# Performance work log

Hardware: AMD Instinct MI355X
Metric: run time of the kernel (lower is better)

The kernel has to match this reference:

```python
import jax, jax.numpy as jnp
import numpy as np

# Model dims (see init_kwargs)
B, S, H = 1, 1024, 2048
NH, NKV, HD = 16, 4, 128       # query heads, kv heads (GQA), head dim
RD = 64                        # partial rotary dim
E, TOPK, I = 8, 2, 1024        # experts, top-k, expert intermediate
EPS = 1e-6
THETA = 1000000.0


def setup_inputs() -> dict:
    key = jax.random.key(0)
    ks = jax.random.split(key, 12)
    s = 0.02  # init scale
    return {
        "hidden_states": jax.random.normal(ks[0], (B, S, H), jnp.float32),
        "position_ids": jnp.tile(jnp.arange(S, dtype=jnp.int32), (B, 1)),
        "ln1_w": jnp.ones((H,), jnp.float32),
        "q_norm_w": jnp.ones((NH * HD,), jnp.float32),
        "k_norm_w": jnp.ones((NKV * HD,), jnp.float32),
        "wq": jax.random.normal(ks[1], (H, NH * HD), jnp.float32) * s,
        "wk": jax.random.normal(ks[2], (H, NKV * HD), jnp.float32) * s,
        "wv": jax.random.normal(ks[3], (H, NKV * HD), jnp.float32) * s,
        "wo": jax.random.normal(ks[4], (NH * HD, H), jnp.float32) * s,
        "ln2_w": jnp.ones((H,), jnp.float32),
        "router_w": jax.random.normal(ks[5], (H, E), jnp.float32) * s,
        "router_bias": jax.random.normal(ks[6], (E,), jnp.float32) * 0.1,
        "w_gate": jax.random.normal(ks[7], (E, H, I), jnp.float32) * s,
        "w_up": jax.random.normal(ks[8], (E, H, I), jnp.float32) * s,
        "w_down": jax.random.normal(ks[9], (E, I, H), jnp.float32) * s,
    }


def rmsnorm(x, w):
    # fp32 RMSNorm over full last dim (matches DistributedRMSNorm with tp=1)
    xf = x.astype(jnp.float32)
    r = jax.lax.rsqrt(jnp.mean(xf * xf, axis=-1, keepdims=True) + EPS)
    return (xf * r * w).astype(x.dtype)


def _rope(x, cos, sin):
    # partial rotary: only first RD dims of each head are rotated
    xr, xp = x[..., :RD], x[..., RD:]
    half = RD // 2
    rot = jnp.concatenate([-xr[..., half:], xr[..., :half]], axis=-1)
    return jnp.concatenate([xr * cos + rot * sin, xp], axis=-1)


def reference(hidden_states, position_ids, ln1_w, q_norm_w, k_norm_w,
              wq, wk, wv, wo, ln2_w, router_w, router_bias,
              w_gate, w_up, w_down):
    x = hidden_states
    # --- attention block ---
    h = rmsnorm(x, ln1_w)
    Q = h @ wq  # [B,S,NH*HD]
    K = h @ wk  # [B,S,NKV*HD]
    V = h @ wv
    # MiniMax M2 qk_norm: RMSNorm over FULL projection output BEFORE head reshape
    Q = rmsnorm(Q, q_norm_w)
    K = rmsnorm(K, k_norm_w)
    q = Q.reshape(B, S, NH, HD).transpose(0, 2, 1, 3)   # [B,NH,S,HD]
    k = K.reshape(B, S, NKV, HD).transpose(0, 2, 1, 3)  # [B,NKV,S,HD]
    v = V.reshape(B, S, NKV, HD).transpose(0, 2, 1, 3)
    # partial RoPE
    inv = 1.0 / (THETA ** (jnp.arange(0, RD, 2, dtype=jnp.float32) / RD))
    ang = position_ids.astype(jnp.float32)[:, :, None] * inv  # [B,S,RD/2]
    cos = jnp.concatenate([jnp.cos(ang)] * 2, axis=-1)[:, None]  # [B,1,S,RD]
    sin = jnp.concatenate([jnp.sin(ang)] * 2, axis=-1)[:, None]
    q = _rope(q, cos, sin)
    k = _rope(k, cos, sin)
    # GQA expand
    rep = NH // NKV
    k = jnp.repeat(k, rep, axis=1)
    v = jnp.repeat(v, rep, axis=1)
    scores = jnp.einsum('bhqd,bhkd->bhqk', q, k).astype(jnp.float32) / np.sqrt(HD).astype(np.float32)
    causal = jnp.tril(jnp.ones((S, S), bool))
    scores = jnp.where(causal, scores, jnp.float32(-1e30))
    attn = jax.nn.softmax(scores, axis=-1).astype(v.dtype)
    ctx = jnp.einsum('bhqk,bhkd->bhqd', attn, v)
    attn_out = ctx.transpose(0, 2, 1, 3).reshape(B, S, NH * HD) @ wo
    res = x + attn_out
    # --- MoE block ---
    h2 = rmsnorm(res, ln2_w)
    t = h2.reshape(B * S, H)
    logits = t.astype(jnp.float32) @ router_w        # [T,E]
    sc = jax.nn.sigmoid(logits)
    # top-k chosen on bias-corrected scores; weights from uncorrected scores
    _, ti = jax.lax.top_k(sc + router_bias, TOPK)    # [T,TOPK]
    aff = jnp.take_along_axis(sc, ti, axis=-1)
    aff = aff / jnp.sum(aff, axis=-1, keepdims=True)  # normalize_top_k_affinities
    T = B * S
    combine = jnp.zeros((T, E), jnp.float32).at[jnp.arange(T)[:, None], ti].add(aff)
    # SwiGLU experts (dense-compute, sparse-combine reference for blockwise grouped GEMM)
    g = jnp.einsum('th,ehi->tei', t, w_gate)
    u = jnp.einsum('th,ehi->tei', t, w_up)
    act = jax.nn.silu(g) * u
    eo = jnp.einsum('tei,eih->teh', act, w_down)
    moe = jnp.einsum('te,teh->th', combine.astype(eo.dtype), eo)
    return res + moe.reshape(B, S, H)
```

## Files before the change

kernel.cpp:

```cpp
#include <hip/hip_runtime.h>
#include <hip/hip_bf16.h>
#include <cstdint>

static constexpr int S   = 1024;
static constexpr int H   = 2048;
static constexpr int NH  = 16;
static constexpr int NKV = 4;
static constexpr int HD  = 128;
static constexpr int EXPN = 8;
static constexpr int FFI = 1024;

typedef __bf16 bf16x8 __attribute__((ext_vector_type(8)));
typedef float  f32x4  __attribute__((ext_vector_type(4)));
typedef unsigned short ushortx8 __attribute__((ext_vector_type(8)));

#define DEVI __device__ __forceinline__

DEVI unsigned short f2bf(float f) {
    union { float f; uint32_t u; } v; v.f = f;
    uint32_t r = (v.u + 0x7FFFu + ((v.u >> 16) & 1u)) >> 16;
    return (unsigned short)r;
}
DEVI float bf2f(unsigned short s) {
    union { uint32_t u; float f; } v; v.u = ((uint32_t)s) << 16; return v.f;
}

DEVI void atomAdd(float* p, float v) { unsafeAtomicAdd(p, v); }

DEVI void gll16(const unsigned short* g, unsigned short* l) {
    __builtin_amdgcn_global_load_lds(
        (const __attribute__((address_space(1))) unsigned int*)(g),
        (__attribute__((address_space(3))) unsigned int*)(l),
        16, 0, 0);
}

__global__ __launch_bounds__(256) void transT(const float* __restrict__ in,
                                              unsigned short* __restrict__ outp,
                                              int R, int C)
{
    __shared__ unsigned short tl[64][72];
    int zb = blockIdx.z;
    in   += (size_t)zb * R * C;
    outp += (size_t)zb * R * C;
    int c0 = blockIdx.x * 64, r0 = blockIdx.y * 64;
    int t = threadIdx.x;
    int cq = (t & 15) * 4;
    int rr = t >> 4;
    #pragma unroll
    for (int p = 0; p < 4; ++p) {
        int row = rr + p * 16;
        float4 v = *(const float4*)&in[(size_t)(r0 + row) * C + c0 + cq];
        tl[cq + 0][row] = f2bf(v.x);
        tl[cq + 1][row] = f2bf(v.y);
        tl[cq + 2][row] = f2bf(v.z);
        tl[cq + 3][row] = f2bf(v.w);
    }
    __syncthreads();
    int r8 = (t & 7) * 8;
    int cc = t >> 3;
    #pragma unroll
    for (int p = 0; p < 2; ++p) {
        int col = cc + p * 32;
        ushortx8 v = *(const ushortx8*)&tl[col][r8];
        *(ushortx8*)&outp[(size_t)(c0 + col) * R + r0 + r8] = v;
    }
}

enum { CFG_PROJ3 = 0, CFG_WO = 1, CFG_SCORES = 2, CFG_PV = 3, CFG_GATEUP = 4, CFG_DOWN = 5 };

template<int CFG, int WM, int NI>
__global__ __launch_bounds__(256, 2) void gemm_k(
    const unsigned short* __restrict__ A,
    const unsigned short* __restrict__ B0,
    const unsigned short* __restrict__ B1,
    const unsigned short* __restrict__ B2,
    float* __restrict__ C0,
    float* __restrict__ C1,
    float* __restrict__ C2,
    unsigned short* __restrict__ Cb,
    const float* __restrict__ X,
    const int* __restrict__ cnt,
    const int* __restrict__ tokList,
    int arg0)
{
    constexpr bool DUAL = (CFG == CFG_GATEUP);
    constexpr int BM = WM * 32;
    constexpr int BN = NI * 32;
    constexpr int ASZ = BM * 64;
    constexpr int BSZ = BN * 64;

    const int tid = threadIdx.x;
    const int m0 = blockIdx.y * BM;
    int n0 = blockIdx.x * BN;

    int M = S;
    int kbeg = 0, kend = 0, LDA = 0, LDBK = 0, LDC = 0;
    const unsigned short* Ap = A;
    const unsigned short* Bb = B0;
    const unsigned short* Bb2 = B1;
    const int* tlist = nullptr;
    float* Cout = C0;
    int head = 0, e = 0, hl = 0;

    if constexpr (CFG == CFG_PROJ3) {
        int xt = blockIdx.x;
        if (xt < 16)      { Bb = B0; Cout = C0; LDC = 2048; n0 = xt * 128; }
        else if (xt < 20) { Bb = B1; Cout = C1; LDC = 512;  n0 = (xt - 16) * 128; }
        else              { Bb = B2; Cout = C2; LDC = 512;  n0 = (xt - 20) * 128; }
        LDA = H; LDBK = H; kend = H;
    } else if constexpr (CFG == CFG_WO) {
        LDA = H; LDBK = H; LDC = H; kend = H;
    } else if constexpr (CFG == CFG_SCORES) {
        hl = blockIdx.z; head = arg0 + hl;
        if (n0 >= m0 + BM) return;
        Ap = A + (size_t)head * S * HD;
        Bb = B0 + (size_t)(head >> 2) * S * HD;
        kend = HD; LDA = HD; LDBK = HD;
    } else if constexpr (CFG == CFG_PV) {
        int z = blockIdx.z; hl = z >> 2; int ks = z & 3;
        head = arg0 + hl;
        int kcap = m0 + BM;
        kbeg = ks * 256;
        if (kbeg >= kcap) return;
        kend = (kbeg + 256 < kcap) ? kbeg + 256 : kcap;
        Ap = A + (size_t)hl * S * S;
        Bb = B0 + (size_t)(head >> 2) * HD * S;
        LDA = S; LDBK = S;
    } else if constexpr (CFG == CFG_GATEUP) {
        e = blockIdx.z;
        M = cnt[e]; if (m0 >= M) return;
        tlist = tokList + e * S;
        Bb  = B0 + (size_t)e * FFI * H;
        Bb2 = B1 + (size_t)e * FFI * H;
        kend = H; LDA = H; LDBK = H;
    } else {
        e = blockIdx.z;
        M = cnt[e]; if (m0 >= M) return;
        Ap = A + (size_t)e * S * FFI;
        Bb = B0 + (size_t)e * H * FFI;
        kend = FFI; LDA = FFI; LDBK = FFI;
    }

    __shared__ unsigned short As[2 * ASZ];
    __shared__ unsigned short Bs[2 * BSZ];
    __shared__ unsigned short Bs2[DUAL ? 2 * BSZ : 8];

    const int lane = tid & 63, grp = lane >> 4, r16 = lane & 15;
    const int wid = tid >> 6, wr = wid >> 1, wc = wid & 1;
    const int wbase8 = (tid & 0xFFC0) * 8;

    size_t aoff[WM];
    #pragma unroll
    for (int c = 0; c < WM; ++c) {
        int chunk = c * 256 + tid;
        int row = chunk >> 3;
        int kcs = (chunk & 7) * 8;
        int grow = m0 + row;
        if constexpr (CFG == CFG_GATEUP) { int r2 = grow < M ? grow : M - 1; grow = tlist[r2]; }
        else if constexpr (CFG == CFG_DOWN) { grow = grow < M ? grow : M - 1; }
        aoff[c] = (size_t)grow * LDA + (kcs ^ ((row & 7) << 3));
    }
    size_t boff[NI];
    #pragma unroll
    for (int c = 0; c < NI; ++c) {
        int chunk = c * 256 + tid;
        int row = chunk >> 3;
        int kcs = (chunk & 7) * 8;
        boff[c] = (size_t)(n0 + row) * LDBK + (kcs ^ ((row & 7) << 3));
    }

    auto STAGE = [&](int buf, int k0) {
        #pragma unroll
        for (int c = 0; c < WM; ++c)
            gll16(Ap + aoff[c] + k0, &As[buf * ASZ + c * 2048 + wbase8]);
        #pragma unroll
        for (int c = 0; c < NI; ++c)
            gll16(Bb + boff[c] + k0, &Bs[buf * BSZ + c * 2048 + wbase8]);
        if constexpr (DUAL) {
            #pragma unroll
            for (int c = 0; c < NI; ++c)
                gll16(Bb2 + boff[c] + k0, &Bs2[buf * BSZ + c * 2048 + wbase8]);
        }
    };

    f32x4 acc[WM][NI] = {};
    f32x4 acc2[DUAL ? WM : 1][DUAL ? NI : 1] = {};

    int cur = 0;
    STAGE(0, kbeg);
    __syncthreads();

    for (int k0 = kbeg; k0 < kend; k0 += 64) {
        if (k0 + 64 < kend) STAGE(cur ^ 1, k0 + 64);
        #pragma unroll
        for (int kk = 0; kk < 64; kk += 32) {
            bf16x8 af[WM], bfr[NI], bfr2[DUAL ? NI : 1];
            #pragma unroll
            for (int mi = 0; mi < WM; ++mi) {
                int r = wr * (WM * 16) + mi * 16 + r16;
                int idx = cur * ASZ + r * 64 + ((kk + grp * 8) ^ ((r & 7) << 3));
                af[mi] = __builtin_bit_cast(bf16x8, *(const ushortx8*)&As[idx]);
            }
            #pragma unroll
            for (int ni = 0; ni < NI; ++ni) {
                int r = wc * (NI * 16) + ni * 16 + r16;
                int idx = cur * BSZ + r * 64 + ((kk + grp * 8) ^ ((r & 7) << 3));
                bfr[ni] = __builtin_bit_cast(bf16x8, *(const ushortx8*)&Bs[idx]);
                if constexpr (DUAL)
                    bfr2[ni] = __builtin_bit_cast(bf16x8, *(const ushortx8*)&Bs2[idx]);
            }
            #pragma unroll
            for (int mi = 0; mi < WM; ++mi)
                #pragma unroll
                for (int ni = 0; ni < NI; ++ni) {
                    acc[mi][ni] = __builtin_amdgcn_mfma_f32_16x16x32_bf16(af[mi], bfr[ni], acc[mi][ni], 0, 0, 0);
                    if constexpr (DUAL)
                        acc2[mi][ni] = __builtin_amdgcn_mfma_f32_16x16x32_bf16(af[mi], bfr2[ni], acc2[mi][ni], 0, 0, 0);
                }
        }
        __syncthreads();
        cur ^= 1;
    }

    #pragma unroll
    for (int mi = 0; mi < WM; ++mi) {
        #pragma unroll
        for (int ni = 0; ni < NI; ++ni) {
            f32x4 v = acc[mi][ni];
            int col = n0 + wc * (NI * 16) + ni * 16 + r16;
            #pragma unroll
            for (int j = 0; j < 4; ++j) {
                int row = m0 + wr * (WM * 16) + mi * 16 + grp * 4 + j;
                float val = v[j];
                if constexpr (CFG == CFG_PROJ3) {
                    Cout[(size_t)row * LDC + col] = val;
                } else if constexpr (CFG == CFG_WO) {
                    C0[(size_t)row * H + col] = val + X[(size_t)row * H + col];
                } else if constexpr (CFG == CFG_SCORES) {
                    float sv = val * 0.08838834764831845f;
                    if (col > row) sv = -1e30f;
                    C0[((size_t)hl * S + row) * S + col] = sv;
                } else if constexpr (CFG == CFG_PV) {
                    atomAdd(&C0[(size_t)row * 2048 + head * HD + col], val);
                } else if constexpr (CFG == CFG_GATEUP) {
                    if (row < M) {
                        float g = val, u = acc2[mi][ni][j];
                        float a = g / (1.f + expf(-g)) * u;
                        Cb[((size_t)e * S + row) * FFI + col] = f2bf(a);
                    }
                } else {
                    if (row < M) {
                        Cb[((size_t)e * S + row) * H + col] = f2bf(val);
                    }
                }
            }
        }
    }
}

__global__ __launch_bounds__(256) void rms_h(const float* __restrict__ x,
                                             const float* __restrict__ w,
                                             unsigned short* __restrict__ out)
{
    int row = blockIdx.x, tid = threadIdx.x;
    const float* xr = x + (size_t)row * H;
    float4 a = *(const float4*)&xr[tid * 8];
    float4 b = *(const float4*)&xr[tid * 8 + 4];
    float vals[8] = { a.x, a.y, a.z, a.w, b.x, b.y, b.z, b.w };
    float ss = 0;
    #pragma unroll
    for (int j = 0; j < 8; ++j) ss += vals[j] * vals[j];
    __shared__ float red[4];
    #pragma unroll
    for (int o = 32; o; o >>= 1) ss += __shfl_down(ss, o);
    if ((tid & 63) == 0) red[tid >> 6] = ss;
    __syncthreads();
    float tot = red[0] + red[1] + red[2] + red[3];
    float r = rsqrtf(tot * (1.f / H) + 1e-6f);
    ushortx8 ov;
    #pragma unroll
    for (int j = 0; j < 8; ++j) ov[j] = f2bf(vals[j] * r * w[tid * 8 + j]);
    *(ushortx8*)&out[(size_t)row * H + tid * 8] = ov;
}

__global__ __launch_bounds__(256) void qnorm_rope(const float* __restrict__ qbuf,
                                                  const float* __restrict__ qw,
                                                  const int* __restrict__ pos,
                                                  unsigned short* __restrict__ qatt)
{
    int tok = blockIdx.x, tid = threadIdx.x;
    __shared__ float sh[2048];
    __shared__ float red[4];
    const float* xr = qbuf + (size_t)tok * 2048;
    float4 a = *(const float4*)&xr[tid * 8];
    float4 b = *(const float4*)&xr[tid * 8 + 4];
    *(float4*)&sh[tid * 8] = a;
    *(float4*)&sh[tid * 8 + 4] = b;
    float ss = a.x*a.x + a.y*a.y + a.z*a.z + a.w*a.w + b.x*b.x + b.y*b.y + b.z*b.z + b.w*b.w;
    #pragma unroll
    for (int o = 32; o; o >>= 1) ss += __shfl_down(ss, o);
    if ((tid & 63) == 0) red[tid >> 6] = ss;
    __syncthreads();
    float tot = red[0] + red[1] + red[2] + red[3];
    float r = rsqrtf(tot * (1.f / 2048.f) + 1e-6f);
    float p = (float)pos[tok];
    #pragma unroll
    for (int j = 0; j < 8; ++j) {
        int idx = tid * 8 + j;
        int d = idx & 127, hh = idx >> 7;
        float v = sh[idx] * r * qw[idx];
        float o;
        if (d < 64) {
            int jj = d & 31;
            float ang = p * expf((float)jj * -0.43173470268f);
            float c = cosf(ang), sn = sinf(ang);
            if (d < 32) { float v2 = sh[idx + 32] * r * qw[idx + 32]; o = v * c - v2 * sn; }
            else        { float v2 = sh[idx - 32] * r * qw[idx - 32]; o = v * c + v2 * sn; }
        } else o = v;
        qatt[((size_t)hh * S + tok) * HD + d] = f2bf(o);
    }
}

__global__ __launch_bounds__(256) void knorm_rope(const float* __restrict__ kbuf,
                                                  const float* __restrict__ kw,
                                                  const int* __restrict__ pos,
                                                  unsigned short* __restrict__ katt)
{
    int tok = blockIdx.x, tid = threadIdx.x;
    __shared__ float sh[512];
    __shared__ float red[4];
    const float* xr = kbuf + (size_t)tok * 512;
    float2 a = *(const float2*)&xr[tid * 2];
    sh[tid * 2] = a.x; sh[tid * 2 + 1] = a.y;
    float ss = a.x * a.x + a.y * a.y;
    #pragma unroll
    for (int o = 32; o; o >>= 1) ss += __shfl_down(ss, o);
    if ((tid & 63) == 0) red[tid >> 6] = ss;
    __syncthreads();
    float tot = red[0] + red[1] + red[2] + red[3];
    float r = rsqrtf(tot * (1.f / 512.f) + 1e-6f);
    float p = (float)pos[tok];
    #pragma unroll
    for (int j = 0; j < 2; ++j) {
        int idx = tid * 2 + j;
        int d = idx & 127, hh = idx >> 7;
        float v = sh[idx] * r * kw[idx];
        float o;
        if (d < 64) {
            int jj = d & 31;
            float ang = p * expf((float)jj * -0.43173470268f);
            float c = cosf(ang), sn = sinf(ang);
            if (d < 32) { float v2 = sh[idx + 32] * r * kw[idx + 32]; o = v * c - v2 * sn; }
            else        { float v2 = sh[idx - 32] * r * kw[idx - 32]; o = v * c + v2 * sn; }
        } else o = v;
        katt[((size_t)hh * S + tok) * HD + d] = f2bf(o);
    }
}

__global__ __launch_bounds__(256) void softmax_k(const float* __restrict__ scores,
                                                 unsigned short* __restrict__ pb)
{
    int bid = blockIdx.x;
    int hl = bid >> 10, q = bid & 1023;
    const float* srow = scores + ((size_t)hl * S + q) * S;
    unsigned short* prow = pb + ((size_t)hl * S + q) * S;
    int L = q + 1, tid = threadIdx.x;
    __shared__ float red[4];
    float v[4]; float mx = -3.4e38f;
    #pragma unroll
    for (int i = 0; i < 4; ++i) {
        int j = tid + i * 256;
        if (j < L) { v[i] = srow[j]; mx = fmaxf(mx, v[i]); } else v[i] = 0.f;
    }
    float m = mx;
    #pragma unroll
    for (int o = 32; o; o >>= 1) m = fmaxf(m, __shfl_down(m, o));
    if ((tid & 63) == 0) red[tid >> 6] = m;
    __syncthreads();
    float M_ = fmaxf(fmaxf(red[0], red[1]), fmaxf(red[2], red[3]));
    __syncthreads();
    float e[4]; float sum = 0;
    #pragma unroll
    for (int i = 0; i < 4; ++i) {
        int j = tid + i * 256;
        if (j < L) { e[i] = expf(v[i] - M_); sum += e[i]; } else e[i] = 0.f;
    }
    #pragma unroll
    for (int o = 32; o; o >>= 1) sum += __shfl_down(sum, o);
    if ((tid & 63) == 0) red[tid >> 6] = sum;
    __syncthreads();
    float inv = 1.f / (red[0] + red[1] + red[2] + red[3]);
    #pragma unroll
    for (int i = 0; i < 4; ++i) {
        int j = tid + i * 256;
        prow[j] = f2bf(e[i] * inv);
    }
}

__global__ void zero_cnt(int* cnt) { if (threadIdx.x < EXPN) cnt[threadIdx.x] = 0; }

__global__ void zerok(float4* __restrict__ p, int n4)
{
    int i = blockIdx.x * 256 + threadIdx.x;
    if (i < n4) p[i] = float4{0.f, 0.f, 0.f, 0.f};
}

__global__ void cvt_k(const float* __restrict__ src, unsigned short* __restrict__ dst)
{
    int i = blockIdx.x * 256 + threadIdx.x;
    float4 a = *(const float4*)&src[i * 8];
    float4 b = *(const float4*)&src[i * 8 + 4];
    float v[8] = { a.x, a.y, a.z, a.w, b.x, b.y, b.z, b.w };
    ushortx8 o;
    #pragma unroll
    for (int j = 0; j < 8; ++j) o[j] = f2bf(v[j]);
    *(ushortx8*)&dst[i * 8] = o;
}

__global__ __launch_bounds__(256) void router_k(const float* __restrict__ res,
                                                const float* __restrict__ ln2w,
                                                const float* __restrict__ rw,
                                                const float* __restrict__ rbias,
                                                int* __restrict__ cnt,
                                                int* __restrict__ tokList,
                                                int* __restrict__ slot,
                                                float* __restrict__ slotw)
{
    int tok = blockIdx.x, tid = threadIdx.x;
    const float* xr = res + (size_t)tok * H;
    float4 a = *(const float4*)&xr[tid * 8];
    float4 b = *(const float4*)&xr[tid * 8 + 4];
    float vals[8] = { a.x, a.y, a.z, a.w, b.x, b.y, b.z, b.w };
    float ss = 0;
    #pragma unroll
    for (int j = 0; j < 8; ++j) ss += vals[j] * vals[j];
    __shared__ float red[4];
    float t_ = ss;
    #pragma unroll
    for (int o = 32; o; o >>= 1) t_ += __shfl_down(t_, o);
    if ((tid & 63) == 0) red[tid >> 6] = t_;
    __syncthreads();
    float tot = red[0] + red[1] + red[2] + red[3];
    float r = rsqrtf(tot * (1.f / H) + 1e-6f);

    float acc[EXPN] = {};
    #pragma unroll
    for (int j = 0; j < 8; ++j) {
        float tv = vals[j] * r * ln2w[tid * 8 + j];
        const float* rp = rw + (size_t)(tid * 8 + j) * EXPN;
        #pragma unroll
        for (int e = 0; e < EXPN; ++e) acc[e] += tv * rp[e];
    }
    __shared__ float r8[4][EXPN];
    #pragma unroll
    for (int e = 0; e < EXPN; ++e) {
        float s_ = acc[e];
        #pragma unroll
        for (int o = 32; o; o >>= 1) s_ += __shfl_down(s_, o);
        acc[e] = s_;
    }
    if ((tid & 63) == 0)
        for (int e = 0; e < EXPN; ++e) r8[tid >> 6][e] = acc[e];
    __syncthreads();
    if (tid == 0) {
        float sg[EXPN];
        for (int e = 0; e < EXPN; ++e) {
            float lg = r8[0][e] + r8[1][e] + r8[2][e] + r8[3][e];
            sg[e] = 1.f / (1.f + expf(-lg));
        }
        int i0 = 0; float b0 = -1e30f;
        for (int e = 0; e < EXPN; ++e) {
            float s_ = sg[e] + rbias[e];
            if (s_ > b0) { b0 = s_; i0 = e; }
        }
        int i1 = -1; float b1 = -1e30f;
        for (int e = 0; e < EXPN; ++e) {
            if (e == i0) continue;
            float s_ = sg[e] + rbias[e];
            if (s_ > b1) { b1 = s_; i1 = e; }
        }
        float a0 = sg[i0], a1 = sg[i1], inv = 1.f / (a0 + a1);
        int p0 = atomicAdd(&cnt[i0], 1);
        tokList[i0 * S + p0] = tok;
        int p1 = atomicAdd(&cnt[i1], 1);
        tokList[i1 * S + p1] = tok;
        slot[tok * 2]     = i0 * S + p0;  slotw[tok * 2]     = a0 * inv;
        slot[tok * 2 + 1] = i1 * S + p1;  slotw[tok * 2 + 1] = a1 * inv;
    }
}

__global__ __launch_bounds__(256) void combine_k(const unsigned short* __restrict__ eo,
                                                 const int* __restrict__ slot,
                                                 const float* __restrict__ slotw,
                                                 float* __restrict__ out)
{
    int t = blockIdx.x;
    int c = threadIdx.x * 8;
    int s0 = slot[t * 2], s1 = slot[t * 2 + 1];
    float w0 = slotw[t * 2], w1 = slotw[t * 2 + 1];
    ushortx8 a = *(const ushortx8*)&eo[(size_t)s0 * H + c];
    ushortx8 b = *(const ushortx8*)&eo[(size_t)s1 * H + c];
    size_t base = (size_t)t * H + c;
    float4 o0 = *(float4*)&out[base];
    float4 o1 = *(float4*)&out[base + 4];
    float ov[8] = { o0.x, o0.y, o0.z, o0.w, o1.x, o1.y, o1.z, o1.w };
    #pragma unroll
    for (int j = 0; j < 8; ++j)
        ov[j] += w0 * bf2f(a[j]) + w1 * bf2f(b[j]);
    *(float4*)&out[base]     = float4{ ov[0], ov[1], ov[2], ov[3] };
    *(float4*)&out[base + 4] = float4{ ov[4], ov[5], ov[6], ov[7] };
}

extern "C" void kernel_launch(void* const* d_in, const int* in_sizes, int n_in,
                              void* d_out, int out_size, void* d_ws, size_t ws_size,
                              hipStream_t stream)
{
    const float* x     = (const float*)d_in[0];
    const int*   pos   = (const int*)d_in[1];
    const float* ln1w  = (const float*)d_in[2];
    const float* qnw   = (const float*)d_in[3];
    const float* knw   = (const float*)d_in[4];
    const float* wq    = (const float*)d_in[5];
    const float* wk    = (const float*)d_in[6];
    const float* wv    = (const float*)d_in[7];
    const float* wo    = (const float*)d_in[8];
    const float* ln2w  = (const float*)d_in[9];
    const float* rw    = (const float*)d_in[10];
    const float* rbias = (const float*)d_in[11];
    const float* wg    = (const float*)d_in[12];
    const float* wu    = (const float*)d_in[13];
    const float* wd    = (const float*)d_in[14];
    float* out = (float*)d_out;

    char* ws = (char*)d_ws;
    const size_t MB = 1024 * 1024;
    unsigned short* h_bf = (unsigned short*)(ws + 0);
    float* qbuf  = (float*)(ws + 4 * MB);
    float* ctxf  = (float*)(ws + 4 * MB);
    float* kbuf  = (float*)(ws + 12 * MB);
    float* vbuf  = (float*)(ws + 14 * MB);
    unsigned short* qatt = (unsigned short*)(ws + 16 * MB);
    unsigned short* katt = (unsigned short*)(ws + 20 * MB);
    unsigned short* vT   = (unsigned short*)(ws + 21 * MB);
    unsigned short* ctx  = (unsigned short*)(ws + 22 * MB);
    unsigned short* tbf  = (unsigned short*)(ws + 26 * MB);
    int*   cnt     = (int*)(ws + 30 * MB);
    int*   tokList = (int*)(ws + 30 * MB + 4096);
    int*   slot    = (int*)(ws + 30 * MB + 512 * 1024);
    float* slotw   = (float*)(ws + 30 * MB + 768 * 1024);
    float* scores = (float*)(ws + 31 * MB);
    unsigned short* pbuf = (unsigned short*)(ws + 63 * MB);
    unsigned short* act = (unsigned short*)(ws + 31 * MB);
    unsigned short* eo  = (unsigned short*)(ws + 47 * MB);
    unsigned short* wqT = (unsigned short*)(ws + 79 * MB);
    unsigned short* wkT = (unsigned short*)(ws + 87 * MB);
    unsigned short* wvT = (unsigned short*)(ws + 89 * MB);
    unsigned short* woT = (unsigned short*)(ws + 91 * MB);
    unsigned short* wgT = (unsigned short*)(ws + 99 * MB);
    unsigned short* wuT = (unsigned short*)(ws + 131 * MB);
    unsigned short* wdT = (unsigned short*)(ws + 163 * MB);

    transT<<<dim3(32, 32, 1), 256, 0, stream>>>(wq, wqT, 2048, 2048);
    transT<<<dim3(8,  32, 1), 256, 0, stream>>>(wk, wkT, 2048, 512);
    transT<<<dim3(8,  32, 1), 256, 0, stream>>>(wv, wvT, 2048, 512);
    transT<<<dim3(32, 32, 1), 256, 0, stream>>>(wo, woT, 2048, 2048);
    transT<<<dim3(16, 32, 8), 256, 0, stream>>>(wg, wgT, 2048, 1024);
    transT<<<dim3(16, 32, 8), 256, 0, stream>>>(wu, wuT, 2048, 1024);
    transT<<<dim3(32, 16, 8), 256, 0, stream>>>(wd, wdT, 1024, 2048);

    rms_h<<<S, 256, 0, stream>>>(x, ln1w, h_bf);

    gemm_k<CFG_PROJ3, 2, 4><<<dim3(24, 16, 1), 256, 0, stream>>>(h_bf, wqT, wkT, wvT, qbuf, kbuf, vbuf, nullptr, nullptr, nullptr, nullptr, 0);

    qnorm_rope<<<S, 256, 0, stream>>>(qbuf, qnw, pos, qatt);
    knorm_rope<<<S, 256, 0, stream>>>(kbuf, knw, pos, katt);
    transT<<<dim3(8, 16, 1), 256, 0, stream>>>(vbuf, vT, 1024, 512);
    zerok<<<2048, 256, 0, stream>>>((float4*)ctxf, (8 * MB) / 16);

    for (int hc = 0; hc < 2; ++hc) {
        gemm_k<CFG_SCORES, 2, 4><<<dim3(8, 16, 8), 256, 0, stream>>>(qatt, katt, nullptr, nullptr, scores, nullptr, nullptr, nullptr, nullptr, nullptr, nullptr, hc * 8);
        softmax_k<<<8 * S, 256, 0, stream>>>(scores, pbuf);
        gemm_k<CFG_PV, 2, 4><<<dim3(1, 16, 32), 256, 0, stream>>>(pbuf, vT, nullptr, nullptr, ctxf, nullptr, nullptr, nullptr, nullptr, nullptr, nullptr, hc * 8);
    }
    cvt_k<<<(S * 2048) / (256 * 8), 256, 0, stream>>>(ctxf, ctx);

    gemm_k<CFG_WO, 2, 4><<<dim3(16, 16, 1), 256, 0, stream>>>(ctx, woT, nullptr, nullptr, out, nullptr, nullptr, nullptr, x, nullptr, nullptr, 0);

    rms_h<<<S, 256, 0, stream>>>(out, ln2w, tbf);
    zero_cnt<<<1, 64, 0, stream>>>(cnt);
    router_k<<<S, 256, 0, stream>>>(out, ln2w, rw, rbias, cnt, tokList, slot, slotw);

    gemm_k<CFG_GATEUP, 2, 2><<<dim3(16, 16, EXPN), 256, 0, stream>>>(tbf, wgT, wuT, nullptr, nullptr, nullptr, nullptr, act, nullptr, cnt, tokList, 0);
    gemm_k<CFG_DOWN, 2, 2><<<dim3(32, 16, EXPN), 256, 0, stream>>>(act, wdT, nullptr, nullptr, nullptr, nullptr, nullptr, eo, nullptr, cnt, tokList, 0);
    combine_k<<<S, 256, 0, stream>>>(eo, slot, slotw, out);
}
```

Before: 377.4 us.

## Triple-buffer GEMM shared-memory stages with explicit vmcnt waits

Replaces the double-buffered K loop in the templated MFMA GEMM with a three-stage ring buffer. Two tiles are prefetched ahead, and the loop waits only on the older stage's global_load_lds via partial s_waitcnt vmcnt counts before a raw s_barrier. This is meant to hide more global-load latency behind MFMA work and avoid the full drain that __syncthreads implies. The cost is 1.5x the LDS footprint, which may reduce occupancy, especially for the dual gate/up config.

```diff
diff --git a/kernel.cpp b/kernel.cpp
--- a/kernel.cpp
+++ b/kernel.cpp
@@ -32,6 +32,19 @@
         (const __attribute__((address_space(1))) unsigned int*)(g),
         (__attribute__((address_space(3))) unsigned int*)(l),
         16, 0, 0);
+}
+
+template<int N> DEVI void waitvm() {
+    if constexpr (N == 0)      asm volatile("s_waitcnt vmcnt(0)" ::: "memory");
+    else if constexpr (N == 2) asm volatile("s_waitcnt vmcnt(2)" ::: "memory");
+    else if constexpr (N == 4) asm volatile("s_waitcnt vmcnt(4)" ::: "memory");
+    else if constexpr (N == 6) asm volatile("s_waitcnt vmcnt(6)" ::: "memory");
+    else static_assert(N == 0 || N == 2 || N == 4 || N == 6, "unsupported vmcnt");
+}
+DEVI void pipe_barrier() {
+    __builtin_amdgcn_sched_barrier(0);
+    __builtin_amdgcn_s_barrier();
+    __builtin_amdgcn_sched_barrier(0);
 }
 
 __global__ __launch_bounds__(256) void transT(const float* __restrict__ in,
@@ -88,6 +101,7 @@
     constexpr int BN = NI * 32;
     constexpr int ASZ = BM * 64;
     constexpr int BSZ = BN * 64;
+    constexpr int LD = WM + NI + (DUAL ? NI : 0);
 
     const int tid = threadIdx.x;
     const int m0 = blockIdx.y * BM;
@@ -141,9 +155,9 @@
         kend = FFI; LDA = FFI; LDBK = FFI;
     }
 
-    __shared__ unsigned short As[2 * ASZ];
-    __shared__ unsigned short Bs[2 * BSZ];
-    __shared__ unsigned short Bs2[DUAL ? 2 * BSZ : 8];
+    __shared__ unsigned short As[3 * ASZ];
+    __shared__ unsigned short Bs[3 * BSZ];
+    __shared__ unsigned short Bs2[DUAL ? 3 * BSZ : 8];
 
     const int lane = tid & 63, grp = lane >> 4, r16 = lane & 15;
     const int wid = tid >> 6, wr = wid >> 1, wc = wid & 1;
@@ -186,25 +200,20 @@
     f32x4 acc[WM][NI] = {};
     f32x4 acc2[DUAL ? WM : 1][DUAL ? NI : 1] = {};
 
-    int cur = 0;
-    STAGE(0, kbeg);
-    __syncthreads();
-
-    for (int k0 = kbeg; k0 < kend; k0 += 64) {
-        if (k0 + 64 < kend) STAGE(cur ^ 1, k0 + 64);
+    auto COMPUTE = [&](int buf) {
         #pragma unroll
         for (int kk = 0; kk < 64; kk += 32) {
             bf16x8 af[WM], bfr[NI], bfr2[DUAL ? NI : 1];
             #pragma unroll
             for (int mi = 0; mi < WM; ++mi) {
                 int r = wr * (WM * 16) + mi * 16 + r16;
-                int idx = cur * ASZ + r * 64 + ((kk + grp * 8) ^ ((r & 7) << 3));
+                int idx = buf * ASZ + r * 64 + ((kk + grp * 8) ^ ((r & 7) << 3));
                 af[mi] = __builtin_bit_cast(bf16x8, *(const ushortx8*)&As[idx]);
             }
             #pragma unroll
             for (int ni = 0; ni < NI; ++ni) {
                 int r = wc * (NI * 16) + ni * 16 + r16;
-                int idx = cur * BSZ + r * 64 + ((kk + grp * 8) ^ ((r & 7) << 3));
+                int idx = buf * BSZ + r * 64 + ((kk + grp * 8) ^ ((r & 7) << 3));
                 bfr[ni] = __builtin_bit_cast(bf16x8, *(const ushortx8*)&Bs[idx]);
                 if constexpr (DUAL)
                     bfr2[ni] = __builtin_bit_cast(bf16x8, *(const ushortx8*)&Bs2[idx]);
@@ -218,8 +227,28 @@
                         acc2[mi][ni] = __builtin_amdgcn_mfma_f32_16x16x32_bf16(af[mi], bfr2[ni], acc2[mi][ni], 0, 0, 0);
                 }
         }
-        __syncthreads();
-        cur ^= 1;
+    };
+
+    const int nk = (kend - kbeg) >> 6;
+
+    STAGE(0, kbeg);
+    if (nk > 1) STAGE(1, kbeg + 64);
+    if (nk > 1) waitvm<LD>(); else waitvm<0>();
+    pipe_barrier();
+
+    int cur = 0, stg = 2;
+    for (int i = 0; i < nk; ++i) {
+        if (i + 2 < nk) {
+            STAGE(stg, kbeg + (i + 2) * 64);
+            stg = (stg == 2) ? 0 : stg + 1;
+        }
+        COMPUTE(cur);
+        cur = (cur == 2) ? 0 : cur + 1;
+        if (i + 1 < nk) {
+            if (i + 2 < nk) waitvm<LD>();
+            else            waitvm<0>();
+            pipe_barrier();
+        }
     }
 
     #pragma unroll
```

Result: no change. 383.7 us (+1.7%).

## Store attention scores in bf16 and process all heads in one pass in place

Applied to the files above, without the earlier changes.

The scores GEMM now writes masked, scaled scores as bf16 instead of fp32. Softmax runs in place on that bf16 buffer with vectorized 4-wide loads and stores. Because the score buffer is half the size, all 16 heads fit in workspace, so the two-chunk loop becomes single launches with larger grids. This cuts score memory traffic and launch count, at the cost of rounding the pre-softmax logits to bf16 and reusing the same buffer for probabilities.

```diff
diff --git a/kernel.cpp b/kernel.cpp
--- a/kernel.cpp
+++ b/kernel.cpp
@@ -13,6 +13,7 @@
 typedef __bf16 bf16x8 __attribute__((ext_vector_type(8)));
 typedef float  f32x4  __attribute__((ext_vector_type(4)));
 typedef unsigned short ushortx8 __attribute__((ext_vector_type(8)));
+typedef unsigned short ushortx4 __attribute__((ext_vector_type(4)));
 
 #define DEVI __device__ __forceinline__
 
@@ -239,7 +240,7 @@
                 } else if constexpr (CFG == CFG_SCORES) {
                     float sv = val * 0.08838834764831845f;
                     if (col > row) sv = -1e30f;
-                    C0[((size_t)hl * S + row) * S + col] = sv;
+                    Cb[((size_t)hl * S + row) * S + col] = f2bf(sv);
                 } else if constexpr (CFG == CFG_PV) {
                     atomAdd(&C0[(size_t)row * 2048 + head * HD + col], val);
                 } else if constexpr (CFG == CFG_GATEUP) {
@@ -357,20 +358,20 @@
     }
 }
 
-__global__ __launch_bounds__(256) void softmax_k(const float* __restrict__ scores,
-                                                 unsigned short* __restrict__ pb)
+__global__ __launch_bounds__(256) void softmax_k(unsigned short* __restrict__ sc)
 {
     int bid = blockIdx.x;
     int hl = bid >> 10, q = bid & 1023;
-    const float* srow = scores + ((size_t)hl * S + q) * S;
-    unsigned short* prow = pb + ((size_t)hl * S + q) * S;
+    unsigned short* srow = sc + ((size_t)hl * S + q) * S;
     int L = q + 1, tid = threadIdx.x;
     __shared__ float red[4];
+    ushortx4 in4 = *(const ushortx4*)&srow[tid * 4];
     float v[4]; float mx = -3.4e38f;
     #pragma unroll
     for (int i = 0; i < 4; ++i) {
-        int j = tid + i * 256;
-        if (j < L) { v[i] = srow[j]; mx = fmaxf(mx, v[i]); } else v[i] = 0.f;
+        int j = tid * 4 + i;
+        if (j < L) { v[i] = bf2f(in4[i]); mx = fmaxf(mx, v[i]); }
+        else v[i] = -3.4e38f;
     }
     float m = mx;
     #pragma unroll
@@ -382,7 +383,7 @@
     float e[4]; float sum = 0;
     #pragma unroll
     for (int i = 0; i < 4; ++i) {
-        int j = tid + i * 256;
+        int j = tid * 4 + i;
         if (j < L) { e[i] = expf(v[i] - M_); sum += e[i]; } else e[i] = 0.f;
     }
     #pragma unroll
@@ -390,11 +391,10 @@
     if ((tid & 63) == 0) red[tid >> 6] = sum;
     __syncthreads();
     float inv = 1.f / (red[0] + red[1] + red[2] + red[3]);
-    #pragma unroll
-    for (int i = 0; i < 4; ++i) {
-        int j = tid + i * 256;
-        prow[j] = f2bf(e[i] * inv);
-    }
+    ushortx4 o4;
+    #pragma unroll
+    for (int i = 0; i < 4; ++i) o4[i] = f2bf(e[i] * inv);
+    *(ushortx4*)&srow[tid * 4] = o4;
 }
 
 __global__ void zero_cnt(int* cnt) { if (threadIdx.x < EXPN) cnt[threadIdx.x] = 0; }
@@ -548,8 +548,7 @@
     int*   tokList = (int*)(ws + 30 * MB + 4096);
     int*   slot    = (int*)(ws + 30 * MB + 512 * 1024);
     float* slotw   = (float*)(ws + 30 * MB + 768 * 1024);
-    float* scores = (float*)(ws + 31 * MB);
-    unsigned short* pbuf = (unsigned short*)(ws + 63 * MB);
+    unsigned short* scores = (unsigned short*)(ws + 31 * MB);
     unsigned short* act = (unsigned short*)(ws + 31 * MB);
     unsigned short* eo  = (unsigned short*)(ws + 47 * MB);
     unsigned short* wqT = (unsigned short*)(ws + 79 * MB);
@@ -577,11 +576,9 @@
     transT<<<dim3(8, 16, 1), 256, 0, stream>>>(vbuf, vT, 1024, 512);
     zerok<<<2048, 256, 0, stream>>>((float4*)ctxf, (8 * MB) / 16);
 
-    for (int hc = 0; hc < 2; ++hc) {
-        gemm_k<CFG_SCORES, 2, 4><<<dim3(8, 16, 8), 256, 0, stream>>>(qatt, katt, nullptr, nullptr, scores, nullptr, nullptr, nullptr, nullptr, nullptr, nullptr, hc * 8);
-        softmax_k<<<8 * S, 256, 0, stream>>>(scores, pbuf);
-        gemm_k<CFG_PV, 2, 4><<<dim3(1, 16, 32), 256, 0, stream>>>(pbuf, vT, nullptr, nullptr, ctxf, nullptr, nullptr, nullptr, nullptr, nullptr, nullptr, hc * 8);
-    }
+    gemm_k<CFG_SCORES, 2, 4><<<dim3(8, 16, 16), 256, 0, stream>>>(qatt, katt, nullptr, nullptr, nullptr, nullptr, nullptr, scores, nullptr, nullptr, nullptr, 0);
+    softmax_k<<<16 * S, 256, 0, stream>>>(scores);
+    gemm_k<CFG_PV, 2, 4><<<dim3(1, 16, 64), 256, 0, stream>>>(scores, vT, nullptr, nullptr, ctxf, nullptr, nullptr, nullptr, nullptr, nullptr, nullptr, 0);
     cvt_k<<<(S * 2048) / (256 * 8), 256, 0, stream>>>(ctxf, ctx);
 
     gemm_k<CFG_WO, 2, 4><<<dim3(16, 16, 1), 256, 0, stream>>>(ctx, woT, nullptr, nullptr, out, nullptr, nullptr, nullptr, x, nullptr, nullptr, 0);
```

New measurement: 367.8 us. 2.6% less time.
